# Performance work log

Measured on AMD Instinct MI355X. Metric: run time of the kernel, lower is better.

## Reference

```python
import jax, jax.numpy as jnp
import numpy as np

B, S, D = 2, 2048, 1024
H, DK = 16, 64            # n_heads, d_k = d_model // n_heads
EXP = 4                   # pattern-separation expand_factor
ED = DK * EXP             # expanded_dim = 256
TOPK = 32                 # top-k kept after ReLU expansion
ALPHA = 0.05
TNT = 1.0                 # trace_norm_target


def setup_inputs() -> dict:
    key = jax.random.key(0)
    ks = jax.random.split(key, 8)
    sc = 1.0 / np.sqrt(D)
    x = jax.random.normal(ks[0], (B, S, D), jnp.float32)
    W_q = jax.random.normal(ks[1], (D, D), jnp.float32) * sc
    W_k = jax.random.normal(ks[2], (D, D), jnp.float32) * sc
    W_v = jax.random.normal(ks[3], (D, D), jnp.float32) * sc
    W_o = jax.random.normal(ks[4], (D, D), jnp.float32) * sc
    # trace buffers (non-zero so the trace read path actually matters)
    traces = jax.random.normal(ks[5], (H, DK, DK), jnp.float32) * 0.02
    value_traces = jax.random.normal(ks[6], (H, ED, DK), jnp.float32) * 0.02
    # frozen random expansion projection (dentate gyrus), W / sqrt(d_k)
    W_expand = jax.random.normal(ks[7], (DK, ED), jnp.float32) / np.sqrt(DK)
    return dict(x=x, W_q=W_q, W_k=W_k, W_v=W_v, W_o=W_o,
                traces=traces, value_traces=value_traces, W_expand=W_expand)


def _eff_alpha(T):
    # alpha / (1 + ||T_h||_F / trace_norm_target), shape (1, H, 1, 1)
    norms = jnp.sqrt(jnp.sum(T * T, axis=(1, 2)))
    return (ALPHA / (1.0 + norms / TNT)).reshape(1, -1, 1, 1)


def _forward(x, W_q, W_k, W_v, W_o, traces, value_traces, W_expand):
    b, s, d = x.shape
    def proj(W):
        return jnp.einsum('bsd,de->bse', x, W).reshape(b, s, H, DK).transpose(0, 2, 1, 3)
    Q, K, V = proj(W_q), proj(W_k), proj(W_v)  # (B, H, S, DK)

    scores = jnp.einsum('bhqd,bhkd->bhqk', Q, K)
    # score trace bias: alpha_eff * (Q @ T @ K^T)
    QT = jnp.einsum('bhqd,hde->bhqe', Q, traces)
    trace_scores = jnp.einsum('bhqe,bhke->bhqk', QT, K)
    scores = (scores + _eff_alpha(traces) * trace_scores) / np.sqrt(DK)
    A = jax.nn.softmax(scores, axis=-1)
    out = jnp.einsum('bhqk,bhkd->bhqd', A, V)

    # value trace read with use_key_q shift: address with previous token's Q
    Q_addr = jnp.concatenate([jnp.zeros_like(Q[:, :, :1, :]), Q[:, :, :-1, :]], axis=2)
    # pattern separation: frozen random expansion + ReLU + top-k sparsify
    Q_exp = jax.nn.relu(jnp.einsum('bhsd,de->bhse', Q_addr, W_expand))  # (B,H,S,ED)
    kth = jax.lax.top_k(Q_exp, TOPK)[0][..., -1:]
    Q_sparse = jnp.where(Q_exp >= kth, Q_exp, 0.0)  # == scatter of top-k vals (ties at 0 contribute 0)
    stored = jnp.einsum('bhse,hed->bhsd', Q_sparse, value_traces)
    out = out + _eff_alpha(value_traces) * stored

    out = out.transpose(0, 2, 1, 3).reshape(b, s, d)
    return jnp.einsum('bsd,de->bse', out, W_o)


def reference(x, W_q, W_k, W_v, W_o, traces, value_traces, W_expand):
    return _forward(x, W_q, W_k, W_v, W_o, traces, value_traces, W_expand)
```

## Files before the change

kernel.cpp:

```cpp
#include <hip/hip_runtime.h>
#include <stdint.h>

#define Bn 2
#define Sn 2048
#define Dn 1024
#define Hn 16
#define DKn 64
#define EDn 256

typedef __attribute__((ext_vector_type(8))) short bvec8;
typedef __attribute__((ext_vector_type(4))) float fvec4;

#define MFMA(a, b, c) __builtin_amdgcn_mfma_f32_16x16x32_bf16(a, b, c, 0, 0, 0)

__device__ __forceinline__ float b2f(unsigned short u) {
  return __uint_as_float(((unsigned)u) << 16);
}
__device__ __forceinline__ unsigned short f2b(float x) {
  unsigned u = __float_as_uint(x);
  u += 0x7fffu + ((u >> 16) & 1u);
  return (unsigned short)(u >> 16);
}
__device__ __forceinline__ void g2l(const unsigned short* g, unsigned short* l) {
  __builtin_amdgcn_global_load_lds(
      (const __attribute__((address_space(1))) void*)g,
      (__attribute__((address_space(3))) void*)l, 16, 0, 0);
}
__device__ __forceinline__ int dpp_sum16(int x) {
  x += __builtin_amdgcn_update_dpp(0, x, 0x140, 0xf, 0xf, true);
  x += __builtin_amdgcn_update_dpp(0, x, 0x141, 0xf, 0xf, true);
  x += __builtin_amdgcn_update_dpp(0, x, 0x1B, 0xf, 0xf, true);
  x += __builtin_amdgcn_update_dpp(0, x, 0xB1, 0xf, 0xf, true);
  return x;
}
__device__ __forceinline__ unsigned dpp_umax16(unsigned x) {
  unsigned t;
  t = (unsigned)__builtin_amdgcn_update_dpp(0, (int)x, 0x140, 0xf, 0xf, true);
  x = x > t ? x : t;
  t = (unsigned)__builtin_amdgcn_update_dpp(0, (int)x, 0x141, 0xf, 0xf, true);
  x = x > t ? x : t;
  t = (unsigned)__builtin_amdgcn_update_dpp(0, (int)x, 0x1B, 0xf, 0xf, true);
  x = x > t ? x : t;
  t = (unsigned)__builtin_amdgcn_update_dpp(0, (int)x, 0xB1, 0xf, 0xf, true);
  x = x > t ? x : t;
  return x;
}

__global__ __launch_bounds__(256) void k_alphas(
    const float* __restrict__ traces, const float* __restrict__ vtr,
    float* __restrict__ alphas) {
  int blk = blockIdx.x;
  const float* base;
  int n;
  if (blk < 16) { base = traces + blk * DKn * DKn; n = DKn * DKn; }
  else          { base = vtr + (blk - 16) * EDn * DKn; n = EDn * DKn; }
  float s = 0.f;
  for (int i = threadIdx.x; i < n; i += 256) { float v = base[i]; s += v * v; }
  __shared__ float red[256];
  red[threadIdx.x] = s;
  __syncthreads();
  for (int off = 128; off > 0; off >>= 1) {
    if (threadIdx.x < off) red[threadIdx.x] += red[threadIdx.x + off];
    __syncthreads();
  }
  if (threadIdx.x == 0) alphas[blk] = 0.05f / (1.f + sqrtf(red[0]));
}

__global__ __launch_bounds__(256) void k_trW(
    const float* __restrict__ w0, const float* __restrict__ w1,
    const float* __restrict__ w2, const float* __restrict__ w3,
    unsigned short* __restrict__ dst) {
  int z = blockIdx.z;
  const float* src = (z == 0) ? w0 : ((z == 1) ? w1 : ((z == 2) ? w2 : w3));
  unsigned short* d = dst + (size_t)z * Dn * Dn;
  __shared__ unsigned short Tl[64][72];
  int tid = threadIdx.x;
  int k0 = blockIdx.y * 64, n0 = blockIdx.x * 64;
#pragma unroll
  for (int i = 0; i < 4; ++i) {
    int q = tid + 256 * i;
    int kr = q >> 4, c4 = q & 15;
    float4 v = *(const float4*)&src[(size_t)(k0 + kr) * Dn + n0 + 4 * c4];
    ushort4 u;
    u.x = f2b(v.x); u.y = f2b(v.y); u.z = f2b(v.z); u.w = f2b(v.w);
    *(ushort4*)&Tl[kr][4 * c4] = u;
  }
  __syncthreads();
#pragma unroll
  for (int i = 0; i < 4; ++i) {
    int q = tid + 256 * i;
    int nr = q >> 4, c4 = q & 15;
    ushort4 u;
    u.x = Tl[4 * c4 + 0][nr]; u.y = Tl[4 * c4 + 1][nr];
    u.z = Tl[4 * c4 + 2][nr]; u.w = Tl[4 * c4 + 3][nr];
    *(ushort4*)&d[(size_t)(n0 + nr) * Dn + k0 + 4 * c4] = u;
  }
}

__global__ __launch_bounds__(256) void k_mkM(const float* __restrict__ tr,
                                             const float* __restrict__ alph,
                                             unsigned short* __restrict__ Mt) {
  int h = blockIdx.x;
  float a = alph[h] * 0.125f;
  const float* th = tr + (size_t)h * DKn * DKn;
  unsigned short* mh = Mt + (size_t)h * DKn * DKn;
  for (int i = threadIdx.x; i < DKn * DKn; i += 256) {
    int e = i >> 6, k = i & 63;
    float v = a * th[(size_t)k * DKn + e] + ((e == k) ? 0.125f : 0.f);
    mh[i] = f2b(v);
  }
}

__global__ __launch_bounds__(256) void k_trE(const float* __restrict__ Wexp,
                                             unsigned short* __restrict__ WexpT) {
  int e0 = blockIdx.x * 64;
  __shared__ unsigned short Tl[64][72];
  int tid = threadIdx.x;
#pragma unroll
  for (int i = 0; i < 4; ++i) {
    int q = tid + 256 * i;
    int dr = q >> 4, c4 = q & 15;
    float4 v = *(const float4*)&Wexp[(size_t)dr * EDn + e0 + 4 * c4];
    ushort4 u;
    u.x = f2b(v.x); u.y = f2b(v.y); u.z = f2b(v.z); u.w = f2b(v.w);
    *(ushort4*)&Tl[dr][4 * c4] = u;
  }
  __syncthreads();
#pragma unroll
  for (int i = 0; i < 4; ++i) {
    int q = tid + 256 * i;
    int er = q >> 4, c4 = q & 15;
    ushort4 u;
    u.x = Tl[4 * c4 + 0][er]; u.y = Tl[4 * c4 + 1][er];
    u.z = Tl[4 * c4 + 2][er]; u.w = Tl[4 * c4 + 3][er];
    *(ushort4*)&WexpT[(size_t)(e0 + er) * DKn + 4 * c4] = u;
  }
}

__global__ __launch_bounds__(256) void k_trVT(const float* __restrict__ vtr,
                                              unsigned short* __restrict__ VTt) {
  int e0 = blockIdx.x * 64;
  int h = blockIdx.y;
  const float* src = vtr + (size_t)h * EDn * DKn;
  unsigned short* dst = VTt + (size_t)h * DKn * EDn;
  __shared__ unsigned short Tl[64][72];
  int tid = threadIdx.x;
#pragma unroll
  for (int i = 0; i < 4; ++i) {
    int q = tid + 256 * i;
    int er = q >> 4, c4 = q & 15;
    float4 v = *(const float4*)&src[(size_t)(e0 + er) * DKn + 4 * c4];
    ushort4 u;
    u.x = f2b(v.x); u.y = f2b(v.y); u.z = f2b(v.z); u.w = f2b(v.w);
    *(ushort4*)&Tl[er][4 * c4] = u;
  }
  __syncthreads();
#pragma unroll
  for (int i = 0; i < 4; ++i) {
    int q = tid + 256 * i;
    int dr = q >> 4, c4 = q & 15;
    ushort4 u;
    u.x = Tl[4 * c4 + 0][dr]; u.y = Tl[4 * c4 + 1][dr];
    u.z = Tl[4 * c4 + 2][dr]; u.w = Tl[4 * c4 + 3][dr];
    *(ushort4*)&dst[(size_t)dr * EDn + e0 + 4 * c4] = u;
  }
}

__global__ __launch_bounds__(256) void k_xb(const float* __restrict__ x,
                                            unsigned short* __restrict__ xb) {
  size_t i = ((size_t)blockIdx.x * 256 + threadIdx.x) * 4;
  float4 v = *(const float4*)&x[i];
  ushort4 u;
  u.x = f2b(v.x); u.y = f2b(v.y); u.z = f2b(v.z); u.w = f2b(v.w);
  *(ushort4*)&xb[i] = u;
}

template <int MODE>
__global__ __launch_bounds__(256) void k_gemm(
    const unsigned short* __restrict__ Ab, const float* __restrict__ Af,
    const unsigned short* __restrict__ BtBase, unsigned short* __restrict__ Qb,
    unsigned short* __restrict__ Kb, unsigned short* __restrict__ VtOut,
    float* __restrict__ Cout) {
  const int z = (MODE == 0) ? blockIdx.z : 0;
  const unsigned short* Bt = BtBase + (size_t)z * Dn * Dn;
  __shared__ unsigned short As[128 * 32];
  __shared__ unsigned short Bs[128 * 32];
  const int tid = threadIdx.x;
  const int w = tid >> 6, lane = tid & 63, qd = lane >> 4, cc = lane & 15;
  const int m0 = blockIdx.y * 128, n0 = blockIdx.x * 128;
  const int mW = 64 * (w >> 1), nW = 64 * (w & 1);
  const int srow = lane >> 2;
  const int schk = 8 * ((lane & 3) ^ (srow & 3));
  const int r0 = 32 * w + srow, r1 = r0 + 16;
  fvec4 acc[4][4];
#pragma unroll
  for (int i = 0; i < 4; ++i)
#pragma unroll
    for (int j = 0; j < 4; ++j) acc[i][j] = (fvec4){0.f, 0.f, 0.f, 0.f};

  for (int k0 = 0; k0 < Dn; k0 += 32) {
    if (MODE == 0) {
      g2l(&Ab[(size_t)(m0 + r0) * Dn + k0 + schk], &As[1024 * w]);
      g2l(&Ab[(size_t)(m0 + r1) * Dn + k0 + schk], &As[1024 * w + 512]);
    } else {
#pragma unroll
      for (int i = 0; i < 4; ++i) {
        int q = tid + 256 * i;
        int row = q >> 3, c4 = q & 7;
        float4 v = *(const float4*)&Af[(size_t)(m0 + row) * Dn + k0 + 4 * c4];
        ushort4 u;
        u.x = f2b(v.x); u.y = f2b(v.y); u.z = f2b(v.z); u.w = f2b(v.w);
        *(ushort4*)&As[row * 32 + 8 * ((c4 >> 1) ^ (row & 3)) + 4 * (c4 & 1)] =
            u;
      }
    }
    g2l(&Bt[(size_t)(n0 + r0) * Dn + k0 + schk], &Bs[1024 * w]);
    g2l(&Bt[(size_t)(n0 + r1) * Dn + k0 + schk], &Bs[1024 * w + 512]);
    __syncthreads();
    bvec8 af[4], bf[4];
#pragma unroll
    for (int i = 0; i < 4; ++i) {
      int ra = mW + 16 * i + cc;
      af[i] = *(const bvec8*)&As[ra * 32 + 8 * (qd ^ (ra & 3))];
      int rb = nW + 16 * i + cc;
      bf[i] = *(const bvec8*)&Bs[rb * 32 + 8 * (qd ^ (rb & 3))];
    }
#pragma unroll
    for (int i = 0; i < 4; ++i)
#pragma unroll
      for (int j = 0; j < 4; ++j) acc[i][j] = MFMA(af[i], bf[j], acc[i][j]);
    __syncthreads();
  }
#pragma unroll
  for (int i = 0; i < 4; ++i)
#pragma unroll
    for (int j = 0; j < 4; ++j) {
      int rowb = m0 + mW + 16 * i + 4 * qd;
      int col = n0 + nW + 16 * j + cc;
      if (MODE == 0) {
        int b = rowb >> 11, s = rowb & 2047;
        int h = col >> 6, dk = col & 63;
        if (z == 2) {
          ushort4 u;
          u.x = f2b(acc[i][j][0]); u.y = f2b(acc[i][j][1]);
          u.z = f2b(acc[i][j][2]); u.w = f2b(acc[i][j][3]);
          *(ushort4*)&VtOut[(((size_t)(b * Hn + h)) * DKn + dk) * Sn + s] = u;
        } else {
          unsigned short* Cb = (z == 0) ? Qb : Kb;
#pragma unroll
          for (int r = 0; r < 4; ++r)
            Cb[(((size_t)(b * Hn + h)) * Sn + s + r) * DKn + dk] =
                f2b(acc[i][j][r]);
        }
      } else {
#pragma unroll
        for (int r = 0; r < 4; ++r)
          Cout[(size_t)(rowb + r) * Dn + col] = acc[i][j][r];
      }
    }
}

__global__ __launch_bounds__(256, 2) void k_pattsep(
    const unsigned short* __restrict__ Qb,
    const unsigned short* __restrict__ WexpT,
    const unsigned short* __restrict__ VTt,
    const float* __restrict__ alphas, float* __restrict__ AT) {
  __shared__ uint4 Wl4[2048];
  __shared__ uint4 Vl4[2048];
  __shared__ uint4 Ps4[4][256];
  const int tile = blockIdx.x, bh = blockIdx.y;
  const int b = bh >> 4, h = bh & 15;
  const int tid = threadIdx.x;
  const int w = tid >> 6, lane = tid & 63, qd = lane >> 4, cc = lane & 15;
  const float avt = alphas[16 + h];

  const uint4* wsrc = (const uint4*)WexpT;
  const uint4* vsrc = (const uint4*)(VTt + (size_t)h * DKn * EDn);
  for (int i = tid; i < 2048; i += 256) {
    int e = i >> 3, c = i & 7;
    Wl4[e * 8 + (c ^ (e & 7))] = wsrc[i];
    int d = i >> 5, c2 = i & 31;
    Vl4[d * 32 + (c2 ^ (d & 7))] = vsrc[i];
  }
  __syncthreads();

  const unsigned short* Wls = (const unsigned short*)Wl4;
  const unsigned short* Vls = (const unsigned short*)Vl4;
  unsigned short* Pw = (unsigned short*)Ps4[w];

  for (int rg = 0; rg < 2; ++rg) {
    const int s0 = tile * 128 + w * 32 + rg * 16;
    bvec8 aq0 = {}, aq1 = {};
    const int srow = s0 + cc;
    if (srow > 0) {
      const unsigned short* qp = Qb + ((size_t)bh * Sn + srow - 1) * DKn;
      aq0 = *(const bvec8*)&qp[8 * qd];
      aq1 = *(const bvec8*)&qp[32 + 8 * qd];
    }
    fvec4 E[16];
#pragma unroll
    for (int j = 0; j < 16; ++j) {
      const int e = 16 * j + cc;
      const unsigned short* wr = Wls + e * 64;
      bvec8 b0 = *(const bvec8*)&wr[8 * (qd ^ (e & 7))];
      bvec8 b1 = *(const bvec8*)&wr[8 * ((4 + qd) ^ (e & 7))];
      fvec4 zv = {0.f, 0.f, 0.f, 0.f};
      zv = MFMA(aq0, b0, zv);
      E[j] = MFMA(aq1, b1, zv);
    }
#pragma unroll
    for (int j = 0; j < 16; ++j)
#pragma unroll
      for (int r = 0; r < 4; ++r) E[j][r] = fmaxf(E[j][r], 0.f);

    float thr[4];
#pragma unroll
    for (int r = 0; r < 4; ++r) {
      unsigned mx = 0u;
#pragma unroll
      for (int j = 0; j < 16; ++j) {
        unsigned e = __float_as_uint(E[j][r]);
        mx = mx > e ? mx : e;
      }
      mx = dpp_umax16(mx);
      {
        unsigned o = (unsigned)__shfl_xor((int)mx, 16);
        mx = mx > o ? mx : o;
        o = (unsigned)__shfl_xor((int)mx, 32);
        mx = mx > o ? mx : o;
      }
      int bstart = (mx == 0u) ? -1 : (31 - __clz((int)mx));
      bstart = __builtin_amdgcn_readfirstlane(bstart);
      unsigned cur = 0u;
      bool done = false;
      for (int bit = bstart; bit >= 0; --bit) {
        unsigned cand = cur | (1u << bit);
        float t = __uint_as_float(cand);
        int cnt = 0;
#pragma unroll
        for (int j = 0; j < 16; ++j) cnt += (E[j][r] >= t) ? 1 : 0;
        cnt = dpp_sum16(cnt);
        if (!done && cnt >= 32) {
          cur = cand;
          if (cnt == 32) done = true;
        }
        if (__all(done)) break;
      }
      thr[r] = __uint_as_float(cur);
    }

    fvec4 acc2[4];
#pragma unroll
    for (int j2 = 0; j2 < 4; ++j2) acc2[j2] = (fvec4){0.f, 0.f, 0.f, 0.f};

#pragma unroll
    for (int half = 0; half < 2; ++half) {
#pragma unroll
      for (int j = 0; j < 8; ++j) {
        const int jj = j + 8 * half;
#pragma unroll
        for (int r = 0; r < 4; ++r) {
          float v = E[jj][r];
          bool sel = (v >= thr[r]) && (v > 0.f);
          int row = 4 * qd + r;
          int s = 16 * j + cc;
          int ch = (s >> 3) ^ (row & 7);
          Pw[row * 128 + ch * 8 + (s & 7)] = sel ? f2b(v) : (unsigned short)0;
        }
      }
#pragma unroll
      for (int j2 = 0; j2 < 4; ++j2) {
        const int d = 16 * j2 + cc;
        const unsigned short* vr = Vls + d * 256;
#pragma unroll
        for (int c = 0; c < 4; ++c) {
          int cg = 4 * (c + 4 * half) + qd;
          bvec8 bv = *(const bvec8*)&vr[8 * (cg ^ (d & 7))];
          int ca = 4 * c + qd;
          bvec8 ap = *(const bvec8*)&Pw[cc * 128 + 8 * (ca ^ (cc & 7))];
          acc2[j2] = MFMA(ap, bv, acc2[j2]);
        }
      }
    }
#pragma unroll
    for (int j2 = 0; j2 < 4; ++j2)
#pragma unroll
      for (int r = 0; r < 4; ++r) {
        int row = s0 + 4 * qd + r;
        AT[((size_t)(b * Sn + row)) * Dn + h * DKn + 16 * j2 + cc] =
            avt * acc2[j2][r];
      }
  }
}

__global__ __launch_bounds__(256, 2) void k_attn(
    const unsigned short* __restrict__ Qb, const unsigned short* __restrict__ Kb,
    const unsigned short* __restrict__ Vt, const unsigned short* __restrict__ Mt,
    float* __restrict__ AT) {
  __shared__ unsigned short Kd[2][64 * 64];
  __shared__ unsigned short Vl[2][64 * 64];
  __shared__ unsigned short Ps[4][32 * 64];
  const int bh = blockIdx.x, qt = blockIdx.y;
  const int b = bh >> 4, h = bh & 15;
  const int tid = threadIdx.x;
  const int w = tid >> 6, lane = tid & 63, qd = lane >> 4, cc = lane & 15;
  const float L2E = 1.4426950408889634f;
  const float NB = 23.083120654223414f;

  const unsigned short* qg = Qb + ((size_t)bh * Sn + qt * 128 + w * 32) * DKn;
  const unsigned short* mh = Mt + (size_t)h * DKn * DKn;
  unsigned short* Pw = Ps[w];
  bvec8 mb0[4], mb1[4];
#pragma unroll
  for (int j = 0; j < 4; ++j) {
    mb0[j] = *(const bvec8*)&mh[(size_t)(16 * j + cc) * DKn + 8 * qd];
    mb1[j] = *(const bvec8*)&mh[(size_t)(16 * j + cc) * DKn + 32 + 8 * qd];
  }
#pragma unroll
  for (int f = 0; f < 2; ++f) {
    bvec8 a0 = *(const bvec8*)&qg[(16 * f + cc) * DKn + 8 * qd];
    bvec8 a1 = *(const bvec8*)&qg[(16 * f + cc) * DKn + 32 + 8 * qd];
#pragma unroll
    for (int j = 0; j < 4; ++j) {
      fvec4 zz = {0.f, 0.f, 0.f, 0.f};
      zz = MFMA(a0, mb0[j], zz);
      zz = MFMA(a1, mb1[j], zz);
#pragma unroll
      for (int r = 0; r < 4; ++r) {
        int qr = 16 * f + 4 * qd + r;
        Pw[qr * 64 + 8 * ((2 * j + (cc >> 3)) ^ (qr & 7)) + (cc & 7)] =
            f2b(zz[r]);
      }
    }
  }
  bvec8 aqA0 = *(const bvec8*)&Pw[cc * 64 + 8 * (qd ^ (cc & 7))];
  bvec8 aqA1 = *(const bvec8*)&Pw[cc * 64 + 8 * ((qd + 4) ^ (cc & 7))];
  bvec8 aqB0 = *(const bvec8*)&Pw[(16 + cc) * 64 + 8 * (qd ^ (cc & 7))];
  bvec8 aqB1 = *(const bvec8*)&Pw[(16 + cc) * 64 + 8 * ((qd + 4) ^ (cc & 7))];

  float lsA = 0.f, lsB = 0.f;
  fvec4 OA[4], OB[4];
#pragma unroll
  for (int j = 0; j < 4; ++j) {
    OA[j] = (fvec4){0.f, 0.f, 0.f, 0.f};
    OB[j] = (fvec4){0.f, 0.f, 0.f, 0.f};
  }

  const int vrow = lane >> 3;
  const int vchk = 8 * ((lane & 7) ^ (vrow & 7));
  const unsigned short* kgb = Kb + (size_t)bh * Sn * DKn;
  const unsigned short* vgb = Vt + (size_t)bh * DKn * Sn;

  g2l(&kgb[(size_t)(16 * w + vrow) * 64 + vchk], &Kd[0][1024 * w]);
  g2l(&kgb[(size_t)(16 * w + 8 + vrow) * 64 + vchk], &Kd[0][1024 * w + 512]);
  g2l(&vgb[(size_t)(16 * w + vrow) * Sn + vchk], &Vl[0][1024 * w]);
  g2l(&vgb[(size_t)(16 * w + 8 + vrow) * Sn + vchk], &Vl[0][1024 * w + 512]);

  const int NT = Sn / 64;
  for (int kt = 0; kt < NT; ++kt) {
    const int buf = kt & 1;
    asm volatile("s_waitcnt vmcnt(0)" ::: "memory");
    __builtin_amdgcn_s_barrier();
    if (kt + 1 < NT) {
      const unsigned short* kg = kgb + (size_t)(kt + 1) * 64 * DKn;
      unsigned short* Kn = Kd[buf ^ 1];
      unsigned short* Vn = Vl[buf ^ 1];
      g2l(&kg[(size_t)(16 * w + vrow) * 64 + vchk], &Kn[1024 * w]);
      g2l(&kg[(size_t)(16 * w + 8 + vrow) * 64 + vchk], &Kn[1024 * w + 512]);
      g2l(&vgb[(size_t)(16 * w + vrow) * Sn + (kt + 1) * 64 + vchk],
          &Vn[1024 * w]);
      g2l(&vgb[(size_t)(16 * w + 8 + vrow) * Sn + (kt + 1) * 64 + vchk],
          &Vn[1024 * w + 512]);
    }
    __builtin_amdgcn_sched_barrier(0);
    const unsigned short* Kc = Kd[buf];
    const unsigned short* Vc = Vl[buf];
    fvec4 sA[4], sB[4];
#pragma unroll
    for (int j = 0; j < 4; ++j) {
      int rk = 16 * j + cc;
      bvec8 b0 = *(const bvec8*)&Kc[rk * 64 + 8 * (qd ^ (cc & 7))];
      bvec8 b1 = *(const bvec8*)&Kc[rk * 64 + 8 * ((qd + 4) ^ (cc & 7))];
      fvec4 z0 = {0.f, 0.f, 0.f, 0.f};
      z0 = MFMA(b0, aqA0, z0);
      sA[j] = MFMA(b1, aqA1, z0);
      fvec4 z1 = {0.f, 0.f, 0.f, 0.f};
      z1 = MFMA(b0, aqB0, z1);
      sB[j] = MFMA(b1, aqB1, z1);
    }
#pragma unroll
    for (int j = 0; j < 4; ++j) {
      float p0 = __builtin_amdgcn_exp2f(fmaf(sA[j][0], L2E, -NB));
      float p1 = __builtin_amdgcn_exp2f(fmaf(sA[j][1], L2E, -NB));
      float p2 = __builtin_amdgcn_exp2f(fmaf(sA[j][2], L2E, -NB));
      float p3 = __builtin_amdgcn_exp2f(fmaf(sA[j][3], L2E, -NB));
      lsA += (p0 + p1) + (p2 + p3);
      unsigned q01, q23;
      asm("v_cvt_pk_bf16_f32 %0, %1, %2" : "=v"(q01) : "v"(p0), "v"(p1));
      asm("v_cvt_pk_bf16_f32 %0, %1, %2" : "=v"(q23) : "v"(p2), "v"(p3));
      uint2 uu;
      uu.x = q01; uu.y = q23;
      *(uint2*)&Pw[cc * 64 + 4 * ((4 * j + qd) ^ cc)] = uu;
    }
#pragma unroll
    for (int j = 0; j < 4; ++j) {
      float p0 = __builtin_amdgcn_exp2f(fmaf(sB[j][0], L2E, -NB));
      float p1 = __builtin_amdgcn_exp2f(fmaf(sB[j][1], L2E, -NB));
      float p2 = __builtin_amdgcn_exp2f(fmaf(sB[j][2], L2E, -NB));
      float p3 = __builtin_amdgcn_exp2f(fmaf(sB[j][3], L2E, -NB));
      lsB += (p0 + p1) + (p2 + p3);
      unsigned q01, q23;
      asm("v_cvt_pk_bf16_f32 %0, %1, %2" : "=v"(q01) : "v"(p0), "v"(p1));
      asm("v_cvt_pk_bf16_f32 %0, %1, %2" : "=v"(q23) : "v"(p2), "v"(p3));
      uint2 uu;
      uu.x = q01; uu.y = q23;
      *(uint2*)&Pw[(16 + cc) * 64 + 4 * ((4 * j + qd) ^ cc)] = uu;
    }
    union U16 { bvec8 v; uint2 u[2]; } UA0, UA1, UB0, UB1;
    UA0.u[0] = *(const uint2*)&Pw[cc * 64 + 4 * ((2 * qd) ^ cc)];
    UA0.u[1] = *(const uint2*)&Pw[cc * 64 + 4 * ((2 * qd + 1) ^ cc)];
    UA1.u[0] = *(const uint2*)&Pw[cc * 64 + 4 * ((8 + 2 * qd) ^ cc)];
    UA1.u[1] = *(const uint2*)&Pw[cc * 64 + 4 * ((9 + 2 * qd) ^ cc)];
    UB0.u[0] = *(const uint2*)&Pw[(16 + cc) * 64 + 4 * ((2 * qd) ^ cc)];
    UB0.u[1] = *(const uint2*)&Pw[(16 + cc) * 64 + 4 * ((2 * qd + 1) ^ cc)];
    UB1.u[0] = *(const uint2*)&Pw[(16 + cc) * 64 + 4 * ((8 + 2 * qd) ^ cc)];
    UB1.u[1] = *(const uint2*)&Pw[(16 + cc) * 64 + 4 * ((9 + 2 * qd) ^ cc)];
#pragma unroll
    for (int j = 0; j < 4; ++j) {
      int rv = 16 * j + cc;
      bvec8 v0 = *(const bvec8*)&Vc[rv * 64 + 8 * (qd ^ (cc & 7))];
      bvec8 v1 = *(const bvec8*)&Vc[rv * 64 + 8 * ((qd + 4) ^ (cc & 7))];
      OA[j] = MFMA(UA0.v, v0, OA[j]);
      OA[j] = MFMA(UA1.v, v1, OA[j]);
      OB[j] = MFMA(UB0.v, v0, OB[j]);
      OB[j] = MFMA(UB1.v, v1, OB[j]);
    }
  }
  lsA += __shfl_xor(lsA, 16);
  lsA += __shfl_xor(lsA, 32);
  lsB += __shfl_xor(lsB, 16);
  lsB += __shfl_xor(lsB, 32);
  float liA = 1.f / lsA, liB = 1.f / lsB;
  float iA[4], iB[4];
#pragma unroll
  for (int r = 0; r < 4; ++r) {
    iA[r] = __shfl(liA, 4 * qd + r);
    iB[r] = __shfl(liB, 4 * qd + r);
  }
#pragma unroll
  for (int j = 0; j < 4; ++j)
#pragma unroll
    for (int r = 0; r < 4; ++r) {
      int rowA = qt * 128 + w * 32 + 4 * qd + r;
      float* pA = AT + ((size_t)(b * Sn + rowA)) * Dn + h * DKn + 16 * j + cc;
      *pA += OA[j][r] * iA[r];
      float* pB = pA + 16 * (size_t)Dn;
      *pB += OB[j][r] * iB[r];
    }
}

extern "C" void kernel_launch(void* const* d_in, const int* in_sizes, int n_in,
                              void* d_out, int out_size, void* d_ws,
                              size_t ws_size, hipStream_t stream) {
  const float* x = (const float*)d_in[0];
  const float* Wq = (const float*)d_in[1];
  const float* Wk = (const float*)d_in[2];
  const float* Wv = (const float*)d_in[3];
  const float* Wo = (const float*)d_in[4];
  const float* traces = (const float*)d_in[5];
  const float* vtr = (const float*)d_in[6];
  const float* Wexp = (const float*)d_in[7];

  const size_t NQ = (size_t)Bn * Hn * Sn * DKn;
  unsigned short* Qb = (unsigned short*)d_ws;
  unsigned short* Kb = Qb + NQ;
  unsigned short* Vt = Kb + NQ;
  unsigned short* Wt = Vt + NQ;
  unsigned short* Mt = Wt + NQ;
  unsigned short* WexpT = Mt + 65536;
  unsigned short* VTt = WexpT + 16384;
  float* alph = (float*)(VTt + 262144);
  float* AT = alph + 32;
  unsigned short* xb = (unsigned short*)AT;

  k_alphas<<<32, 256, 0, stream>>>(traces, vtr, alph);
  k_trW<<<dim3(16, 16, 4), 256, 0, stream>>>(Wq, Wk, Wv, Wo, Wt);
  k_mkM<<<16, 256, 0, stream>>>(traces, alph, Mt);
  k_trE<<<4, 256, 0, stream>>>(Wexp, WexpT);
  k_trVT<<<dim3(4, 16), 256, 0, stream>>>(vtr, VTt);
  k_xb<<<4096, 256, 0, stream>>>(x, xb);
  k_gemm<0><<<dim3(8, 32, 3), 256, 0, stream>>>(xb, nullptr, Wt, Qb, Kb, Vt,
                                                nullptr);
  k_pattsep<<<dim3(16, 32), 256, 0, stream>>>(Qb, WexpT, VTt, alph, AT);
  k_attn<<<dim3(32, 16), 256, 0, stream>>>(Qb, Kb, Vt, Mt, AT);
  k_gemm<1><<<dim3(8, 32, 1), 256, 0, stream>>>(
      nullptr, AT, Wt + 3 * (size_t)Dn * Dn, nullptr, nullptr, nullptr,
      (float*)d_out);
}
```

Measured before the change: 284.9 us.

## Load V directly from global into registers and add MFMA priority hints

Removes the LDS staging buffer for V in the attention kernel. Each wave now loads its V fragments straight from global memory into registers at the start of each key tile, and the K tile stays double-buffered in LDS. It also wraps the MFMA sections in s_setprio to favour matrix work across waves. This cuts LDS traffic and footprint, which may allow more occupancy. In exchange, every wave now issues its own redundant global/L2 loads of V, and those loads are waited on within the same iteration, so their latency is no longer prefetched a tile ahead.

```diff
diff --git a/kernel.cpp b/kernel.cpp
--- a/kernel.cpp
+++ b/kernel.cpp
@@ -398,7 +398,6 @@
     const unsigned short* __restrict__ Vt, const unsigned short* __restrict__ Mt,
     float* __restrict__ AT) {
   __shared__ unsigned short Kd[2][64 * 64];
-  __shared__ unsigned short Vl[2][64 * 64];
   __shared__ unsigned short Ps[4][32 * 64];
   const int bh = blockIdx.x, qt = blockIdx.y;
   const int b = bh >> 4, h = bh & 15;
@@ -453,29 +452,30 @@
 
   g2l(&kgb[(size_t)(16 * w + vrow) * 64 + vchk], &Kd[0][1024 * w]);
   g2l(&kgb[(size_t)(16 * w + 8 + vrow) * 64 + vchk], &Kd[0][1024 * w + 512]);
-  g2l(&vgb[(size_t)(16 * w + vrow) * Sn + vchk], &Vl[0][1024 * w]);
-  g2l(&vgb[(size_t)(16 * w + 8 + vrow) * Sn + vchk], &Vl[0][1024 * w + 512]);
 
   const int NT = Sn / 64;
   for (int kt = 0; kt < NT; ++kt) {
     const int buf = kt & 1;
     asm volatile("s_waitcnt vmcnt(0)" ::: "memory");
     __builtin_amdgcn_s_barrier();
+    bvec8 vr0[4], vr1[4];
+#pragma unroll
+    for (int j = 0; j < 4; ++j) {
+      const unsigned short* vp = &vgb[(size_t)(16 * j + cc) * Sn + kt * 64];
+      vr0[j] = *(const bvec8*)&vp[8 * qd];
+      vr1[j] = *(const bvec8*)&vp[8 * (qd + 4)];
+    }
+    __builtin_amdgcn_sched_barrier(0);
     if (kt + 1 < NT) {
       const unsigned short* kg = kgb + (size_t)(kt + 1) * 64 * DKn;
       unsigned short* Kn = Kd[buf ^ 1];
-      unsigned short* Vn = Vl[buf ^ 1];
       g2l(&kg[(size_t)(16 * w + vrow) * 64 + vchk], &Kn[1024 * w]);
       g2l(&kg[(size_t)(16 * w + 8 + vrow) * 64 + vchk], &Kn[1024 * w + 512]);
-      g2l(&vgb[(size_t)(16 * w + vrow) * Sn + (kt + 1) * 64 + vchk],
-          &Vn[1024 * w]);
-      g2l(&vgb[(size_t)(16 * w + 8 + vrow) * Sn + (kt + 1) * 64 + vchk],
-          &Vn[1024 * w + 512]);
     }
     __builtin_amdgcn_sched_barrier(0);
     const unsigned short* Kc = Kd[buf];
-    const unsigned short* Vc = Vl[buf];
     fvec4 sA[4], sB[4];
+    __builtin_amdgcn_s_setprio(1);
 #pragma unroll
     for (int j = 0; j < 4; ++j) {
       int rk = 16 * j + cc;
@@ -488,6 +488,7 @@
       z1 = MFMA(b0, aqB0, z1);
       sB[j] = MFMA(b1, aqB1, z1);
     }
+    __builtin_amdgcn_s_setprio(0);
 #pragma unroll
     for (int j = 0; j < 4; ++j) {
       float p0 = __builtin_amdgcn_exp2f(fmaf(sA[j][0], L2E, -NB));
@@ -525,16 +526,15 @@
     UB0.u[1] = *(const uint2*)&Pw[(16 + cc) * 64 + 4 * ((2 * qd + 1) ^ cc)];
     UB1.u[0] = *(const uint2*)&Pw[(16 + cc) * 64 + 4 * ((8 + 2 * qd) ^ cc)];
     UB1.u[1] = *(const uint2*)&Pw[(16 + cc) * 64 + 4 * ((9 + 2 * qd) ^ cc)];
-#pragma unroll
-    for (int j = 0; j < 4; ++j) {
-      int rv = 16 * j + cc;
-      bvec8 v0 = *(const bvec8*)&Vc[rv * 64 + 8 * (qd ^ (cc & 7))];
-      bvec8 v1 = *(const bvec8*)&Vc[rv * 64 + 8 * ((qd + 4) ^ (cc & 7))];
-      OA[j] = MFMA(UA0.v, v0, OA[j]);
-      OA[j] = MFMA(UA1.v, v1, OA[j]);
-      OB[j] = MFMA(UB0.v, v0, OB[j]);
-      OB[j] = MFMA(UB1.v, v1, OB[j]);
-    }
+    __builtin_amdgcn_s_setprio(1);
+#pragma unroll
+    for (int j = 0; j < 4; ++j) {
+      OA[j] = MFMA(UA0.v, vr0[j], OA[j]);
+      OA[j] = MFMA(UA1.v, vr1[j], OA[j]);
+      OB[j] = MFMA(UB0.v, vr0[j], OB[j]);
+      OB[j] = MFMA(UB1.v, vr1[j], OB[j]);
+    }
+    __builtin_amdgcn_s_setprio(0);
   }
   lsA += __shfl_xor(lsA, 16);
   lsA += __shfl_xor(lsA, 32);
```

Result: slower. 304.6 us (+6.9%).
